# Optimization experiments

Hardware: AMD Instinct MI355X
Metric: run time of the kernel (lower is better)

## Reference

```python
import jax, jax.numpy as jnp
import numpy as np

N_NODES = 15000
N_EDGES = 30000
NUM_GRAPHS = 600
N_STEMS = 6000
N_JBONDS = 3000
DIM = 64
NUM_FEAT = 14
NUM_OUT_PER_STEM = 105


def _lin(a, w, b):
    return a @ w.T + b


def _forward(x, edge_attr, lin0_w, lin0_b, en1_w, en1_b, en2_w, en2_b, root_w, conv_b,
             gru_w_ih, gru_w_hh, gru_b_ih, gru_b_hh, s1_w, s1_b, s2_w, s2_b,
             j1_w, j1_b, j2_w, j2_b, lstm_w_ih, lstm_w_hh, lstm_b_ih, lstm_b_hh,
             lout_w, lout_b, edge_index, stem_atmidx, jbond_atmidx, batch):
    n, dim = x.shape[0], lin0_w.shape[0]
    lrelu = jax.nn.leaky_relu  # negative_slope=0.01 as in torch default
    src, dst = edge_index[0], edge_index[1]

    out = lrelu(_lin(x, lin0_w, lin0_b))
    h = out  # GRU hidden state [N, dim]

    # Edge-conditioned weights (NNConv): small MLP on edge_attr -> [E, dim, dim]
    We = _lin(lrelu(_lin(edge_attr, en1_w, en1_b)), en2_w, en2_b).reshape(-1, dim, dim)
    deg = jnp.clip(jax.ops.segment_sum(jnp.ones_like(dst, dtype=x.dtype), dst, num_segments=n), 1.0)

    for _ in range(6):
        # gather source features, per-edge matvec, scatter-mean to destinations
        msg = jnp.einsum('ei,eio->eo', out[src], We)
        agg = jax.ops.segment_sum(msg, dst, num_segments=n) / deg[:, None]
        m = lrelu(agg + out @ root_w + conv_b)
        # GRUCell (torch gate order: r, z, n)
        gi = _lin(m, gru_w_ih, gru_b_ih)
        gh = _lin(h, gru_w_hh, gru_b_hh)
        ir, iz, inn = jnp.split(gi, 3, axis=-1)
        hr, hz, hn = jnp.split(gh, 3, axis=-1)
        r = jax.nn.sigmoid(ir + hr)
        z = jax.nn.sigmoid(iz + hz)
        ng = jnp.tanh(inn + r * hn)
        h = (1.0 - z) * ng + z * h
        out = h

    stem_preds = _lin(lrelu(_lin(out[stem_atmidx], s1_w, s1_b)), s2_w, s2_b)
    jb = _lin(lrelu(_lin(out[jbond_atmidx.reshape(-1)], j1_w, j1_b)), j2_w, j2_b)
    jbond_preds = jb.reshape(jbond_atmidx.shape).mean(axis=1)

    # Set2Set with 1 processing step (LSTM input 2*dim -> hidden dim)
    b = NUM_GRAPHS
    q_star = jnp.zeros((b, 2 * dim), x.dtype)
    hl = jnp.zeros((b, dim), x.dtype)
    cl = jnp.zeros((b, dim), x.dtype)
    gates = _lin(q_star, lstm_w_ih, lstm_b_ih) + _lin(hl, lstm_w_hh, lstm_b_hh)
    i_, f_, g_, o_ = jnp.split(gates, 4, axis=-1)  # torch LSTM gate order i,f,g,o
    c = jax.nn.sigmoid(f_) * cl + jax.nn.sigmoid(i_) * jnp.tanh(g_)
    q = jax.nn.sigmoid(o_) * jnp.tanh(c)
    e = (out * q[batch]).sum(axis=-1)  # [N]
    emax = jax.ops.segment_max(e, batch, num_segments=b)
    a_un = jnp.exp(e - emax[batch])
    a = a_un / jax.ops.segment_sum(a_un, batch, num_segments=b)[batch]
    r_pool = jax.ops.segment_sum(a[:, None] * out, batch, num_segments=b)
    q_star = jnp.concatenate([q, r_pool], axis=-1)  # [B, 2*dim]

    final = _lin(q_star, lout_w, lout_b)  # [B, 2]
    return final, stem_preds, jbond_preds


def setup_inputs() -> dict:
    key = jax.random.key(0)
    ks = jax.random.split(key, 40)
    d = DIM

    def rn(k, shape, s=0.1):
        return jax.random.normal(k, shape, dtype=jnp.float32) * s

    inp = {}
    inp['x'] = jax.random.normal(ks[0], (N_NODES, NUM_FEAT), dtype=jnp.float32)
    inp['edge_attr'] = jax.random.uniform(ks[1], (N_EDGES, 4), dtype=jnp.float32)
    inp['lin0_w'] = rn(ks[2], (d, NUM_FEAT)); inp['lin0_b'] = rn(ks[3], (d,))
    inp['en1_w'] = rn(ks[4], (d, 4)); inp['en1_b'] = rn(ks[5], (d,))
    inp['en2_w'] = rn(ks[6], (d * d, d), 0.02); inp['en2_b'] = rn(ks[7], (d * d,), 0.02)
    inp['root_w'] = rn(ks[8], (d, d)); inp['conv_b'] = rn(ks[9], (d,))
    inp['gru_w_ih'] = rn(ks[10], (3 * d, d)); inp['gru_w_hh'] = rn(ks[11], (3 * d, d))
    inp['gru_b_ih'] = rn(ks[12], (3 * d,)); inp['gru_b_hh'] = rn(ks[13], (3 * d,))
    inp['s1_w'] = rn(ks[14], (d, d)); inp['s1_b'] = rn(ks[15], (d,))
    inp['s2_w'] = rn(ks[16], (NUM_OUT_PER_STEM, d)); inp['s2_b'] = rn(ks[17], (NUM_OUT_PER_STEM,))
    inp['j1_w'] = rn(ks[18], (d, d)); inp['j1_b'] = rn(ks[19], (d,))
    inp['j2_w'] = rn(ks[20], (1, d)); inp['j2_b'] = rn(ks[21], (1,))
    inp['lstm_w_ih'] = rn(ks[22], (4 * d, 2 * d)); inp['lstm_w_hh'] = rn(ks[23], (4 * d, d))
    inp['lstm_b_ih'] = rn(ks[24], (4 * d,)); inp['lstm_b_hh'] = rn(ks[25], (4 * d,))
    inp['lout_w'] = rn(ks[26], (2, 2 * d)); inp['lout_b'] = rn(ks[27], (2,))
    inp['edge_index'] = jax.random.randint(ks[28], (2, N_EDGES), 0, N_NODES)
    inp['stem_atmidx'] = jax.random.randint(ks[29], (N_STEMS,), 0, N_NODES)
    inp['jbond_atmidx'] = jax.random.randint(ks[30], (N_JBONDS, 2), 0, N_NODES)
    inp['batch'] = jnp.sort(jax.random.randint(ks[31], (N_NODES,), 0, NUM_GRAPHS))
    return inp


def reference(x, edge_attr, lin0_w, lin0_b, en1_w, en1_b, en2_w, en2_b, root_w, conv_b,
              gru_w_ih, gru_w_hh, gru_b_ih, gru_b_hh, s1_w, s1_b, s2_w, s2_b,
              j1_w, j1_b, j2_w, j2_b, lstm_w_ih, lstm_w_hh, lstm_b_ih, lstm_b_hh,
              lout_w, lout_b, edge_index, stem_atmidx, jbond_atmidx, batch):
    return _forward(x, edge_attr, lin0_w, lin0_b, en1_w, en1_b, en2_w, en2_b, root_w, conv_b,
                    gru_w_ih, gru_w_hh, gru_b_ih, gru_b_hh, s1_w, s1_b, s2_w, s2_b,
                    j1_w, j1_b, j2_w, j2_b, lstm_w_ih, lstm_w_hh, lstm_b_ih, lstm_b_hh,
                    lout_w, lout_b, edge_index, stem_atmidx, jbond_atmidx, batch)
```

## Files before the change

### kernel.cpp

```cpp
#include <hip/hip_runtime.h>

typedef unsigned short u16;
typedef unsigned int   u32;

#define N_NODES    15000
#define PADN       15008
#define N_EDGES    30000
#define NUM_GRAPHS 600
#define N_STEMS    6000
#define N_JBONDS   3000

#define OUT_FINAL  0
#define OUT_STEM   1200
#define OUT_JB     631200

#define A1S 68
#define N_CVT 26

#define EBLK 32
#define EGRIDE 938
#define KCH 130
#define A1LS 66
#define RS   66

#define NGROUPS (PADN/16)
#define NWTILES 28
#define HS 72

typedef short frag8 __attribute__((ext_vector_type(8)));
typedef float facc4 __attribute__((ext_vector_type(4)));

__device__ __forceinline__ float u2f(u16 v){ union{u32 i; float f;} c; c.i=((u32)v)<<16; return c.f; }
__device__ __forceinline__ float blo(u32 x){ union{u32 i; float f;} c; c.i=x<<16; return c.f; }
__device__ __forceinline__ float bhi(u32 x){ union{u32 i; float f;} c; c.i=x&0xffff0000u; return c.f; }
__device__ __forceinline__ u16  f2b(float f){ union{float f; u32 u;} c; c.f=f; u32 u=c.u;
                                              return (u16)((u + 0x7fffu + ((u>>16)&1u))>>16); }
__device__ __forceinline__ float lrelu(float x){ return x>0.f ? x : 0.01f*x; }
__device__ __forceinline__ float sigmoidf(float x){ return 1.f/(1.f+expf(-x)); }

__device__ __forceinline__ int lower_bound_i(const int* __restrict__ a, int n, int v){
  int lo=0, hi=n;
  while(lo<hi){ int m=(lo+hi)>>1; if(a[m]<v) lo=m+1; else hi=m; }
  return lo;
}

__device__ __forceinline__ void store_out(void* dout, int isf, int idx, float v){
  if(isf) ((float*)dout)[idx] = v;
  else    ((u16*)dout)[idx]   = f2b(v);
}

__device__ __forceinline__ frag8 pack4(uint4 v, float av){
  union { u32 d[4]; frag8 f; } au;
  u32 dd0 = v.x, dd1 = v.y, dd2 = v.z, dd3 = v.w;
  {
    float plo = blo(dd0)*av, phi = bhi(dd0)*av;
    au.d[0] = __builtin_amdgcn_perm(__float_as_uint(phi)+0x8000u,
                                    __float_as_uint(plo)+0x8000u, 0x07060302u);
  }
  {
    float plo = blo(dd1)*av, phi = bhi(dd1)*av;
    au.d[1] = __builtin_amdgcn_perm(__float_as_uint(phi)+0x8000u,
                                    __float_as_uint(plo)+0x8000u, 0x07060302u);
  }
  {
    float plo = blo(dd2)*av, phi = bhi(dd2)*av;
    au.d[2] = __builtin_amdgcn_perm(__float_as_uint(phi)+0x8000u,
                                    __float_as_uint(plo)+0x8000u, 0x07060302u);
  }
  {
    float plo = blo(dd3)*av, phi = bhi(dd3)*av;
    au.d[3] = __builtin_amdgcn_perm(__float_as_uint(phi)+0x8000u,
                                    __float_as_uint(plo)+0x8000u, 0x07060302u);
  }
  return au.f;
}

__global__ __launch_bounds__(256) void k_sniff(const u16* __restrict__ x, int n, int* __restrict__ flag){
  int i = blockIdx.x*256 + threadIdx.x;
  int local = 0;
  for(; i < n; i += gridDim.x*256){
    u16 v = x[i];
    if(((v>>7)&0xFFu) == 0xFFu) local = 1;
  }
  if(local) atomicOr(flag, 1);
}

struct CvtArgs { const void* src[N_CVT]; float* dst[N_CVT]; int n[N_CVT]; };

__global__ __launch_bounds__(256) void k_cvt(CvtArgs A, const int* __restrict__ flag){
  int isf = *flag;
  int tid = blockIdx.x*256 + threadIdx.x;
  int stride = gridDim.x*256;
  for(int b=0; b<N_CVT; b++){
    int n = A.n[b];
    const float* sf = (const float*)A.src[b];
    const u16*   sb = (const u16*)A.src[b];
    float* d = A.dst[b];
    for(int i=tid; i<n; i+=stride) d[i] = isf ? sf[i] : u2f(sb[i]);
  }
}

__global__ __launch_bounds__(64) void k_lin0(const float* __restrict__ x, const float* __restrict__ w,
                                             const float* __restrict__ b,
                                             float* __restrict__ outF, u16* __restrict__ outB){
  int n = blockIdx.x, o = threadIdx.x;
  __shared__ float xs[14];
  if(o<14) xs[o] = x[n*14+o];
  __syncthreads();
  float acc = b[o];
  #pragma unroll
  for(int i=0;i<14;i++) acc += xs[i]*w[o*14+i];
  float v = lrelu(acc);
  outF[n*64+o] = v;
  outB[n*64+o] = f2b(v);
}

__global__ __launch_bounds__(128) void k_a1(const float* __restrict__ ea,
                                            const float* __restrict__ en1w, const float* __restrict__ en1b,
                                            u16* __restrict__ a1b){
  int e = blockIdx.x, k = threadIdx.x;
  if(k >= A1S) return;
  float v = 0.f;
  if(k < 64){
    float acc = en1b[k];
    #pragma unroll
    for(int c=0;c<4;c++) acc += ea[e*4+c] * en1w[k*4+c];
    v = lrelu(acc);
  } else if(k == 64) v = 1.0f;
  a1b[e*A1S + k] = f2b(v);
}

__global__ __launch_bounds__(256) void k_packW2b(const float* __restrict__ en2w, const float* __restrict__ en2b,
                                                 u16* __restrict__ B2b){
  int idx = blockIdx.x*256 + threadIdx.x;
  if(idx >= KCH*2048) return;
  int jj  = idx & 7;
  int l   = (idx >> 3) & 63;
  int nt  = (idx >> 9) & 3;
  int c   = idx >> 11;
  int q = l >> 4, m16 = l & 15;
  int kidx = c*32 + q*8 + jj;
  int k = kidx >> 6, j = kidx & 63;
  int o = nt*16 + m16;
  float v = (k < 64) ? en2w[((size_t)(j*64 + o))*64 + k] : en2b[j*64 + o];
  B2b[idx] = f2b(v);
}

__global__ __launch_bounds__(256) void k_packNodeW(const float* __restrict__ rootw, const float* __restrict__ wih,
                                                   const float* __restrict__ whh, u16* __restrict__ gBn){
  int idx = blockIdx.x*256 + threadIdx.x;
  if(idx >= NWTILES*4*512) return;
  int jj = idx & 7, l = (idx>>3) & 63, ch = (idx>>9) & 3, t = idx >> 11;
  int m16 = l & 15, q = l >> 4;
  int j = ((ch & 1) ? 32 : 0) + q*8 + jj;
  float v;
  if(t < 4){        int o = t*16 + m16;        v = rootw[j*64 + o]; }
  else if(t < 16){  int g = (t-4)*16 + m16;    v = wih[(size_t)g*64 + j]; }
  else {            int g = (t-16)*16 + m16;   v = whh[(size_t)g*64 + j]; }
  u16 hb = f2b(v);
  gBn[idx] = (ch >> 1) ? f2b(v - u2f(hb)) : hb;
}

__global__ __launch_bounds__(256) void k_packHeads(const float* __restrict__ s1w, const float* __restrict__ s2w,
                                                   const float* __restrict__ j1w,
                                                   float4* __restrict__ s1P, float4* __restrict__ s2P,
                                                   float4* __restrict__ j1P){
  int idx = blockIdx.x*256 + threadIdx.x;
  if(idx < 1024){
    int o = idx & 63, j4 = idx >> 6;
    const float* r = s1w + o*64 + 4*j4;
    s1P[idx] = (float4){r[0], r[1], r[2], r[3]};
    const float* r2 = j1w + o*64 + 4*j4;
    j1P[idx] = (float4){r2[0], r2[1], r2[2], r2[3]};
  }
  if(idx < 1792){
    int j4 = idx / 112, t = idx % 112;
    float4 v = {0.f,0.f,0.f,0.f};
    if(t < 105){
      const float* r = s2w + t*64 + 4*j4;
      v = (float4){r[0], r[1], r[2], r[3]};
    }
    s2P[idx] = v;
  }
}

__global__ __launch_bounds__(256) void k_deg(const int* __restrict__ dst, float* __restrict__ deg){
  int e = blockIdx.x*256 + threadIdx.x;
  if(e < N_EDGES) atomicAdd(&deg[dst[e]], 1.0f);
}

__global__ __launch_bounds__(256, 4) void k_egemm(const u16* __restrict__ outB,
                                               const u16* __restrict__ a1b,
                                               const u16* __restrict__ B2b,
                                               const int* __restrict__ ei,
                                               float* __restrict__ agg){
  int tid = threadIdx.x;
  int l = tid & 63, w = tid >> 6;
  int m16 = l & 15, q = l >> 4;
  int eb = blockIdx.x * EBLK;

  __shared__ __align__(16) u16 a1l[EBLK*A1LS];
  __shared__ __align__(16) float red[4][EBLK*RS];

  int e0 = eb + m16, e1 = eb + 16 + m16;
  int n0 = (e0 < N_EDGES) ? ei[e0] : 0;
  int n1 = (e1 < N_EDGES) ? ei[e1] : 0;
  uint4 o200 = *(const uint4*)(outB + (size_t)n0*64 +      q*8);
  uint4 o201 = *(const uint4*)(outB + (size_t)n0*64 + 32 + q*8);
  uint4 o210 = *(const uint4*)(outB + (size_t)n1*64 +      q*8);
  uint4 o211 = *(const uint4*)(outB + (size_t)n1*64 + 32 + q*8);

  for(int idx = tid; idx < EBLK*33; idx += 256){
    int r = idx / 33, c = idx - r*33;
    int e = eb + r;
    u32 v = (e < N_EDGES) ? ((const u32*)(a1b + (size_t)e*A1S))[c] : 0u;
    ((u32*)a1l)[r*33 + c] = v;
  }
  __syncthreads();

  facc4 acc[2][4];
  #pragma unroll
  for(int t=0;t<2;t++)
    #pragma unroll
    for(int nt=0;nt<4;nt++) acc[t][nt] = (facc4){0.f,0.f,0.f,0.f};

  int ks = (w*65) >> 2, ke = ((w+1)*65) >> 2;
  const frag8* __restrict__ Bg = (const frag8*)B2b;

  frag8 bA[4], bB[4];
  #pragma unroll
  for(int nt=0;nt<4;nt++) bA[nt] = Bg[(size_t)(2*ks)*256 + nt*64 + l];

  for(int k = ks; k < ke; ++k){
    #pragma unroll
    for(int nt=0;nt<4;nt++) bB[nt] = Bg[(size_t)(2*k+1)*256 + nt*64 + l];

    float av0 = u2f(a1l[m16*A1LS + k]);
    float av1 = u2f(a1l[(16+m16)*A1LS + k]);

    {
      frag8 au0 = pack4(o200, av0);
      frag8 au1 = pack4(o210, av1);
      #pragma unroll
      for(int nt=0;nt<4;nt++)
        acc[0][nt] = __builtin_amdgcn_mfma_f32_16x16x32_bf16(au0, bA[nt], acc[0][nt], 0,0,0);
      #pragma unroll
      for(int nt=0;nt<4;nt++)
        acc[1][nt] = __builtin_amdgcn_mfma_f32_16x16x32_bf16(au1, bA[nt], acc[1][nt], 0,0,0);
    }

    int kn = (k+1 < ke) ? (k+1) : k;
    #pragma unroll
    for(int nt=0;nt<4;nt++) bA[nt] = Bg[(size_t)(2*kn)*256 + nt*64 + l];

    {
      frag8 au0 = pack4(o201, av0);
      frag8 au1 = pack4(o211, av1);
      #pragma unroll
      for(int nt=0;nt<4;nt++)
        acc[0][nt] = __builtin_amdgcn_mfma_f32_16x16x32_bf16(au0, bB[nt], acc[0][nt], 0,0,0);
      #pragma unroll
      for(int nt=0;nt<4;nt++)
        acc[1][nt] = __builtin_amdgcn_mfma_f32_16x16x32_bf16(au1, bB[nt], acc[1][nt], 0,0,0);
    }
  }

  #pragma unroll
  for(int t = 0; t < 2; t++){
    #pragma unroll
    for(int nt = 0; nt < 4; nt++){
      #pragma unroll
      for(int r = 0; r < 4; r++){
        int el = t*16 + q*4 + r;
        red[w][el*RS + nt*16 + m16] = acc[t][nt][r];
      }
    }
  }
  __syncthreads();

  for(int i = tid; i < EBLK*64; i += 256){
    int el = i >> 6, o = i & 63;
    int e = eb + el;
    if(e < N_EDGES){
      float s = red[0][el*RS + o] + red[1][el*RS + o]
              + red[2][el*RS + o] + red[3][el*RS + o];
      atomicAdd(&agg[(size_t)ei[N_EDGES + e]*64 + o], s);
    }
  }
}

__global__ __launch_bounds__(256) void k_node(float* __restrict__ agg, const float* __restrict__ deg,
                                              float* __restrict__ outF, u16* __restrict__ outB,
                                              const u16* __restrict__ gBn, const float* __restrict__ convb,
                                              const float* __restrict__ bih, const float* __restrict__ bhh){
  int tid = threadIdx.x;
  int l = tid & 63, w = tid >> 6;
  int m16 = l & 15, q = l >> 4;
  int nb = blockIdx.x * 16;

  __shared__ __align__(16) u16 hhi[16][HS], hlo[16][HS];
  __shared__ __align__(16) u16 mhi[16][HS], mlo[16][HS];

  {
    float4 v = ((const float4*)(outF + (size_t)nb*64))[tid];
    int base = tid*4;
    int node = base >> 6, o = base & 63;
    float vv[4] = {v.x, v.y, v.z, v.w};
    #pragma unroll
    for(int t=0;t<4;t++){
      u16 hb = f2b(vv[t]);
      hhi[node][o+t] = hb;
      hlo[node][o+t] = f2b(vv[t] - u2f(hb));
    }
  }
  __syncthreads();

  const frag8* __restrict__ Bg = (const frag8*)gBn;

#define GEMM6(ACC, A0, A1, L0, L1, T)                                      \
  {                                                                        \
    const frag8* bp = Bg + (size_t)(T)*256 + l;                            \
    frag8 b0 = bp[0], b1 = bp[64], b2 = bp[128], b3 = bp[192];             \
    ACC = __builtin_amdgcn_mfma_f32_16x16x32_bf16(A0, b0, ACC, 0,0,0);     \
    ACC = __builtin_amdgcn_mfma_f32_16x16x32_bf16(A1, b1, ACC, 0,0,0);     \
    ACC = __builtin_amdgcn_mfma_f32_16x16x32_bf16(L0, b0, ACC, 0,0,0);     \
    ACC = __builtin_amdgcn_mfma_f32_16x16x32_bf16(L1, b1, ACC, 0,0,0);     \
    ACC = __builtin_amdgcn_mfma_f32_16x16x32_bf16(A0, b2, ACC, 0,0,0);     \
    ACC = __builtin_amdgcn_mfma_f32_16x16x32_bf16(A1, b3, ACC, 0,0,0);     \
  }

  frag8 hA0 = *(const frag8*)&hhi[m16][q*8];
  frag8 hA1 = *(const frag8*)&hhi[m16][32 + q*8];
  frag8 hL0 = *(const frag8*)&hlo[m16][q*8];
  frag8 hL1 = *(const frag8*)&hlo[m16][32 + q*8];

  facc4 dR  = (facc4){0.f,0.f,0.f,0.f};
  facc4 ghA = (facc4){0.f,0.f,0.f,0.f};
  facc4 ghB = (facc4){0.f,0.f,0.f,0.f};
  facc4 ghC = (facc4){0.f,0.f,0.f,0.f};
  GEMM6(dR,  hA0, hA1, hL0, hL1, w);
  GEMM6(ghA, hA0, hA1, hL0, hL1, 16 + w);
  GEMM6(ghB, hA0, hA1, hL0, hL1, 20 + w);
  GEMM6(ghC, hA0, hA1, hL0, hL1, 24 + w);

  int o = w*16 + m16;
  float cb = convb[o];
  #pragma unroll
  for(int r=0;r<4;r++){
    int node = q*4 + r;
    int n = nb + node;
    float a = agg[(size_t)n*64 + o] / fmaxf(deg[n], 1.0f) + dR[r] + cb;
    agg[(size_t)n*64 + o] = 0.f;
    float mv = lrelu(a);
    u16 mb = f2b(mv);
    mhi[node][o] = mb;
    mlo[node][o] = f2b(mv - u2f(mb));
  }
  __syncthreads();

  frag8 mA0 = *(const frag8*)&mhi[m16][q*8];
  frag8 mA1 = *(const frag8*)&mhi[m16][32 + q*8];
  frag8 mL0 = *(const frag8*)&mlo[m16][q*8];
  frag8 mL1 = *(const frag8*)&mlo[m16][32 + q*8];

  facc4 giA = (facc4){0.f,0.f,0.f,0.f};
  facc4 giB = (facc4){0.f,0.f,0.f,0.f};
  facc4 giC = (facc4){0.f,0.f,0.f,0.f};
  GEMM6(giA, mA0, mA1, mL0, mL1, 4 + w);
  GEMM6(giB, mA0, mA1, mL0, mL1, 8 + w);
  GEMM6(giC, mA0, mA1, mL0, mL1, 12 + w);
#undef GEMM6

  float bi0 = bih[o], bi1 = bih[64+o], bi2 = bih[128+o];
  float bh0 = bhh[o], bh1 = bhh[64+o], bh2 = bhh[128+o];
  #pragma unroll
  for(int r=0;r<4;r++){
    int node = q*4 + r;
    int n = nb + node;
    float ir = giA[r]+bi0, iz = giB[r]+bi1, inn = giC[r]+bi2;
    float hr = ghA[r]+bh0, hz = ghB[r]+bh1, hn = ghC[r]+bh2;
    float rr  = sigmoidf(ir + hr);
    float z   = sigmoidf(iz + hz);
    float ngv = tanhf(inn + rr*hn);
    float hold = u2f(hhi[node][o]) + u2f(hlo[node][o]);
    float hnew = (1.f - z)*ngv + z*hold;
    if(n < N_NODES){
      outF[(size_t)n*64 + o] = hnew;
      outB[(size_t)n*64 + o] = f2b(hnew);
    }
  }
}

__global__ __launch_bounds__(512) void k_stem(const float* __restrict__ outF, const int* __restrict__ sidx,
                                              const float4* __restrict__ s1P, const float* __restrict__ s1b,
                                              const float4* __restrict__ s2P, const float* __restrict__ s2b,
                                              void* __restrict__ dout, const int* __restrict__ flag){
  int grp = threadIdx.x >> 7, t = threadIdx.x & 127;
  int s = blockIdx.x*4 + grp;
  int isf = *flag;
  __shared__ __align__(16) float xs[4][64], hid[4][64];
  int a = sidx[s];
  if(t < 64) xs[grp][t] = outF[(size_t)a*64 + t];
  __syncthreads();
  if(t < 64){
    float acc = s1b[t];
    const float4* xp = (const float4*)xs[grp];
    #pragma unroll 8
    for(int j4=0;j4<16;j4++){
      float4 w = s1P[j4*64+t];
      float4 x = xp[j4];
      acc += w.x*x.x + w.y*x.y + w.z*x.z + w.w*x.w;
    }
    hid[grp][t] = lrelu(acc);
  }
  __syncthreads();
  if(t < 105){
    float acc = s2b[t];
    const float4* hp = (const float4*)hid[grp];
    #pragma unroll 8
    for(int j4=0;j4<16;j4++){
      float4 w = s2P[j4*112+t];
      float4 h = hp[j4];
      acc += w.x*h.x + w.y*h.y + w.z*h.z + w.w*h.w;
    }
    store_out(dout, isf, OUT_STEM + s*105 + t, acc);
  }
}

__global__ __launch_bounds__(512) void k_jbond(const float* __restrict__ outF, const int* __restrict__ jidx,
                                               const float4* __restrict__ j1P, const float* __restrict__ j1b,
                                               const float* __restrict__ j2w, const float* __restrict__ j2b,
                                               void* __restrict__ dout, const int* __restrict__ flag){
  int grp = threadIdx.x >> 7, t = threadIdx.x & 127;
  int jb = blockIdx.x*4 + grp;
  int isf = *flag;
  __shared__ __align__(16) float xs[4][2][64], hid[4][2][64];
  int at = t >> 6, k = t & 63;
  int a = jidx[jb*2 + at];
  xs[grp][at][k] = outF[(size_t)a*64 + k];
  __syncthreads();
  {
    float acc = j1b[k];
    const float4* xp = (const float4*)xs[grp][at];
    #pragma unroll 8
    for(int j4=0;j4<16;j4++){
      float4 w = j1P[j4*64+k];
      float4 x = xp[j4];
      acc += w.x*x.x + w.y*x.y + w.z*x.z + w.w*x.w;
    }
    hid[grp][at][k] = lrelu(acc);
  }
  __syncthreads();
  if(t < 64){
    float p = (hid[grp][0][t] + hid[grp][1][t]) * j2w[t];
    #pragma unroll
    for(int s=32;s;s>>=1) p += __shfl_xor(p, s, 64);
    if(t==0) store_out(dout, isf, OUT_JB + jb, 0.5f*p + j2b[0]);
  }
}

__global__ __launch_bounds__(64) void k_s2s(const float* __restrict__ outF, const int* __restrict__ batch,
                                            const float* __restrict__ bih, const float* __restrict__ bhh,
                                            const float* __restrict__ loutw, const float* __restrict__ loutb,
                                            void* __restrict__ dout, const int* __restrict__ flag){
  int b = blockIdx.x, t = threadIdx.x;
  int isf = *flag;
  float i_ = bih[t]     + bhh[t];
  float g_ = bih[128+t] + bhh[128+t];
  float o_ = bih[192+t] + bhh[192+t];
  float c  = sigmoidf(i_)*tanhf(g_);
  float q  = sigmoidf(o_)*tanhf(c);

  int lo = lower_bound_i(batch, N_NODES, b);
  int hi = lower_bound_i(batch, N_NODES, b+1);

  float emax = -3.4e38f;
  for(int n=lo;n<hi;n++){
    float p = outF[n*64+t]*q;
    #pragma unroll
    for(int s=32;s;s>>=1) p += __shfl_xor(p, s, 64);
    emax = fmaxf(emax, p);
  }
  float Z = 0.f, racc = 0.f;
  for(int n=lo;n<hi;n++){
    float v = outF[n*64+t];
    float p = v*q;
    #pragma unroll
    for(int s=32;s;s>>=1) p += __shfl_xor(p, s, 64);
    float w = expf(p - emax);
    Z += w; racc += w*v;
  }
  float rp = (hi>lo) ? racc/Z : 0.f;

  #pragma unroll
  for(int j=0;j<2;j++){
    float p = q*loutw[j*128+t] + rp*loutw[j*128+64+t];
    #pragma unroll
    for(int s=32;s;s>>=1) p += __shfl_xor(p, s, 64);
    if(t==0) store_out(dout, isf, OUT_FINAL + b*2 + j, p + loutb[j]);
  }
}

extern "C" void kernel_launch(void* const* d_in, const int* in_sizes, int n_in,
                              void* d_out, int out_size, void* d_ws, size_t ws_size,
                              hipStream_t stream) {
  const int* edge_index  = (const int*)d_in[28];
  const int* stem_atmidx = (const int*)d_in[29];
  const int* jbond_atmidx= (const int*)d_in[30];
  const int* batch       = (const int*)d_in[31];

  char* ws = (char*)d_ws;
  size_t off = 0;
  auto alloc = [&](size_t bytes)->void*{ void* p = ws + off; off = (off + bytes + 255) & ~(size_t)255; return p; };

  int*   flag = (int*)  alloc(4);
  float* outF = (float*)alloc((size_t)PADN*64*4);
  u16*   outB = (u16*)  alloc((size_t)PADN*64*2);
  float* agg  = (float*)alloc((size_t)PADN*64*4);
  u16*   a1b  = (u16*)  alloc((size_t)N_EDGES*A1S*2);
  u16*   B2b  = (u16*)  alloc((size_t)KCH*2048*2 + 2048*2);
  u16*   gBn  = (u16*)  alloc((size_t)NWTILES*4*512*2);
  float* deg  = (float*)alloc((size_t)PADN*4);
  float4* s1P   = (float4*)alloc(1024*16);
  float4* s2P   = (float4*)alloc(1792*16);
  float4* j1P   = (float4*)alloc(1024*16);

  static const int cvt_idx[N_CVT] = {0,1,2,3,4,5,6,7,8,9,10,11,12,13,14,15,16,17,18,19,20,21,24,25,26,27};
  CvtArgs A;
  float* cF[N_CVT];
  for(int i=0;i<N_CVT;i++){
    int src = cvt_idx[i];
    int n = in_sizes[src];
    cF[i] = (float*)alloc((size_t)n*4);
    A.src[i] = d_in[src];
    A.dst[i] = cF[i];
    A.n[i]   = n;
  }
  (void)ws_size; (void)n_in; (void)out_size;
  float* xF=cF[0];   float* eaF=cF[1];  float* l0w=cF[2];  float* l0b=cF[3];
  float* e1w=cF[4];  float* e1b=cF[5];  float* e2w=cF[6];  float* e2b=cF[7];
  float* rootw=cF[8];float* convb=cF[9];
  float* wih=cF[10]; float* whh=cF[11]; float* bih=cF[12]; float* bhh=cF[13];
  float* s1w=cF[14]; float* s1b=cF[15]; float* s2w=cF[16]; float* s2b=cF[17];
  float* j1w=cF[18]; float* j1b=cF[19]; float* j2w=cF[20]; float* j2b=cF[21];
  float* lbih=cF[22];float* lbhh=cF[23];float* loutw=cF[24];float* loutb=cF[25];

  hipMemsetAsync(flag, 0, 4, stream);
  hipMemsetAsync(deg,  0, (size_t)PADN*4, stream);
  hipMemsetAsync(outF + (size_t)N_NODES*64, 0, (size_t)(PADN-N_NODES)*64*4, stream);
  hipMemsetAsync(outB + (size_t)N_NODES*64, 0, (size_t)(PADN-N_NODES)*64*2, stream);
  hipMemsetAsync(agg,  0, (size_t)PADN*64*4, stream);

  k_sniff <<<128, 256, 0, stream>>>((const u16*)d_in[0], in_sizes[0], flag);
  k_cvt   <<<512, 256, 0, stream>>>(A, flag);

  k_lin0    <<<N_NODES, 64, 0, stream>>>(xF, l0w, l0b, outF, outB);
  k_a1      <<<N_EDGES, 128, 0, stream>>>(eaF, e1w, e1b, a1b);
  k_packW2b <<<(KCH*2048+255)/256, 256, 0, stream>>>(e2w, e2b, B2b);
  k_packNodeW<<<(NWTILES*4*512+255)/256, 256, 0, stream>>>(rootw, wih, whh, gBn);
  k_packHeads<<<7, 256, 0, stream>>>(s1w, s2w, j1w, s1P, s2P, j1P);
  k_deg     <<<(N_EDGES+255)/256, 256, 0, stream>>>(edge_index + N_EDGES, deg);

  for(int it=0; it<6; it++){
    k_egemm<<<EGRIDE, 256, 0, stream>>>(outB, a1b, B2b, edge_index, agg);
    k_node <<<NGROUPS, 256, 0, stream>>>(agg, deg, outF, outB, gBn, convb, bih, bhh);
  }

  k_stem <<<N_STEMS/4, 512, 0, stream>>>(outF, stem_atmidx, s1P, s1b, s2P, s2b, d_out, flag);
  k_jbond<<<N_JBONDS/4, 512, 0, stream>>>(outF, jbond_atmidx, j1P, j1b, j2w, j2b, d_out, flag);
  k_s2s  <<<NUM_GRAPHS, 64, 0, stream>>>(outF, batch, lbih, lbhh, loutw, loutb, d_out, flag);
}
```

Before: 457.0 us.

## Merge setup kernels and deepen B-fragment prefetch in the edge GEMM

The buffer memsets are folded into the sniff kernel, the degree count is folded into k_a1, and the three weight-packing kernels become one k_packAll launch. Together these cut the number of separate setup launches. In k_egemm the B-fragment prefetch now loads a whole pair of k-steps ahead, so more loads are in flight per MFMA batch. Launch bounds drop from 4 to 3 blocks per CU to leave room for the extra fragment registers, which may lower occupancy.

```diff
diff --git a/kernel.cpp b/kernel.cpp
--- a/kernel.cpp
+++ b/kernel.cpp
@@ -26,6 +26,11 @@
 #define NGROUPS (PADN/16)
 #define NWTILES 28
 #define HS 72
+
+#define PACK_W2B_N (KCH*2048)
+#define PACK_NW_N  (NWTILES*4*512)
+#define PACK_HD_N  1792
+#define PACK_TOTAL (PACK_W2B_N + PACK_NW_N + PACK_HD_N)
 
 typedef short frag8 __attribute__((ext_vector_type(8)));
 typedef float facc4 __attribute__((ext_vector_type(4)));
@@ -75,14 +80,22 @@
   return au.f;
 }
 
-__global__ __launch_bounds__(256) void k_sniff(const u16* __restrict__ x, int n, int* __restrict__ flag){
-  int i = blockIdx.x*256 + threadIdx.x;
+__global__ __launch_bounds__(256) void k_sniff(const u16* __restrict__ x, int n, int* __restrict__ flag,
+                                               float* __restrict__ deg, float* __restrict__ agg,
+                                               float* __restrict__ outF, u16* __restrict__ outB){
+  int tid = blockIdx.x*256 + threadIdx.x;
+  int stride = gridDim.x*256;
   int local = 0;
-  for(; i < n; i += gridDim.x*256){
+  for(int i = tid; i < n; i += stride){
     u16 v = x[i];
     if(((v>>7)&0xFFu) == 0xFFu) local = 1;
   }
   if(local) atomicOr(flag, 1);
+  float4 z = (float4){0.f,0.f,0.f,0.f};
+  for(int i = tid; i < PADN; i += stride) deg[i] = 0.f;
+  for(int i = tid; i < PADN*64/4; i += stride) ((float4*)agg)[i] = z;
+  for(int i = tid; i < (PADN-N_NODES)*64/4; i += stride) ((float4*)(outF + (size_t)N_NODES*64))[i] = z;
+  for(int i = tid; i < (PADN-N_NODES)*64/8; i += stride) ((float4*)(outB + (size_t)N_NODES*64))[i] = z;
 }
 
 struct CvtArgs { const void* src[N_CVT]; float* dst[N_CVT]; int n[N_CVT]; };
@@ -117,7 +130,8 @@
 
 __global__ __launch_bounds__(128) void k_a1(const float* __restrict__ ea,
                                             const float* __restrict__ en1w, const float* __restrict__ en1b,
-                                            u16* __restrict__ a1b){
+                                            u16* __restrict__ a1b,
+                                            const int* __restrict__ ei, float* __restrict__ deg){
   int e = blockIdx.x, k = threadIdx.x;
   if(k >= A1S) return;
   float v = 0.f;
@@ -128,68 +142,66 @@
     v = lrelu(acc);
   } else if(k == 64) v = 1.0f;
   a1b[e*A1S + k] = f2b(v);
-}
-
-__global__ __launch_bounds__(256) void k_packW2b(const float* __restrict__ en2w, const float* __restrict__ en2b,
-                                                 u16* __restrict__ B2b){
+  if(k == 65) atomicAdd(&deg[ei[N_EDGES + e]], 1.0f);
+}
+
+__global__ __launch_bounds__(256) void k_packAll(const float* __restrict__ en2w, const float* __restrict__ en2b,
+                                                 u16* __restrict__ B2b,
+                                                 const float* __restrict__ rootw, const float* __restrict__ wih,
+                                                 const float* __restrict__ whh, u16* __restrict__ gBn,
+                                                 const float* __restrict__ s1w, const float* __restrict__ s2w,
+                                                 const float* __restrict__ j1w,
+                                                 float4* __restrict__ s1P, float4* __restrict__ s2P,
+                                                 float4* __restrict__ j1P){
   int idx = blockIdx.x*256 + threadIdx.x;
-  if(idx >= KCH*2048) return;
-  int jj  = idx & 7;
-  int l   = (idx >> 3) & 63;
-  int nt  = (idx >> 9) & 3;
-  int c   = idx >> 11;
-  int q = l >> 4, m16 = l & 15;
-  int kidx = c*32 + q*8 + jj;
-  int k = kidx >> 6, j = kidx & 63;
-  int o = nt*16 + m16;
-  float v = (k < 64) ? en2w[((size_t)(j*64 + o))*64 + k] : en2b[j*64 + o];
-  B2b[idx] = f2b(v);
-}
-
-__global__ __launch_bounds__(256) void k_packNodeW(const float* __restrict__ rootw, const float* __restrict__ wih,
-                                                   const float* __restrict__ whh, u16* __restrict__ gBn){
-  int idx = blockIdx.x*256 + threadIdx.x;
-  if(idx >= NWTILES*4*512) return;
-  int jj = idx & 7, l = (idx>>3) & 63, ch = (idx>>9) & 3, t = idx >> 11;
-  int m16 = l & 15, q = l >> 4;
-  int j = ((ch & 1) ? 32 : 0) + q*8 + jj;
-  float v;
-  if(t < 4){        int o = t*16 + m16;        v = rootw[j*64 + o]; }
-  else if(t < 16){  int g = (t-4)*16 + m16;    v = wih[(size_t)g*64 + j]; }
-  else {            int g = (t-16)*16 + m16;   v = whh[(size_t)g*64 + j]; }
-  u16 hb = f2b(v);
-  gBn[idx] = (ch >> 1) ? f2b(v - u2f(hb)) : hb;
-}
-
-__global__ __launch_bounds__(256) void k_packHeads(const float* __restrict__ s1w, const float* __restrict__ s2w,
-                                                   const float* __restrict__ j1w,
-                                                   float4* __restrict__ s1P, float4* __restrict__ s2P,
-                                                   float4* __restrict__ j1P){
-  int idx = blockIdx.x*256 + threadIdx.x;
-  if(idx < 1024){
-    int o = idx & 63, j4 = idx >> 6;
-    const float* r = s1w + o*64 + 4*j4;
-    s1P[idx] = (float4){r[0], r[1], r[2], r[3]};
-    const float* r2 = j1w + o*64 + 4*j4;
-    j1P[idx] = (float4){r2[0], r2[1], r2[2], r2[3]};
-  }
-  if(idx < 1792){
-    int j4 = idx / 112, t = idx % 112;
-    float4 v = {0.f,0.f,0.f,0.f};
-    if(t < 105){
-      const float* r = s2w + t*64 + 4*j4;
-      v = (float4){r[0], r[1], r[2], r[3]};
-    }
-    s2P[idx] = v;
-  }
-}
-
-__global__ __launch_bounds__(256) void k_deg(const int* __restrict__ dst, float* __restrict__ deg){
-  int e = blockIdx.x*256 + threadIdx.x;
-  if(e < N_EDGES) atomicAdd(&deg[dst[e]], 1.0f);
-}
-
-__global__ __launch_bounds__(256, 4) void k_egemm(const u16* __restrict__ outB,
+  if(idx < PACK_W2B_N){
+    int jj  = idx & 7;
+    int l   = (idx >> 3) & 63;
+    int nt  = (idx >> 9) & 3;
+    int c   = idx >> 11;
+    int q = l >> 4, m16 = l & 15;
+    int kidx = c*32 + q*8 + jj;
+    int k = kidx >> 6, j = kidx & 63;
+    int o = nt*16 + m16;
+    float v = (k < 64) ? en2w[((size_t)(j*64 + o))*64 + k] : en2b[j*64 + o];
+    B2b[idx] = f2b(v);
+    return;
+  }
+  idx -= PACK_W2B_N;
+  if(idx < PACK_NW_N){
+    int jj = idx & 7, l = (idx>>3) & 63, ch = (idx>>9) & 3, t = idx >> 11;
+    int m16 = l & 15, q = l >> 4;
+    int j = ((ch & 1) ? 32 : 0) + q*8 + jj;
+    float v;
+    if(t < 4){        int o = t*16 + m16;        v = rootw[j*64 + o]; }
+    else if(t < 16){  int g = (t-4)*16 + m16;    v = wih[(size_t)g*64 + j]; }
+    else {            int g = (t-16)*16 + m16;   v = whh[(size_t)g*64 + j]; }
+    u16 hb = f2b(v);
+    gBn[idx] = (ch >> 1) ? f2b(v - u2f(hb)) : hb;
+    return;
+  }
+  idx -= PACK_NW_N;
+  if(idx < PACK_HD_N){
+    if(idx < 1024){
+      int o = idx & 63, j4 = idx >> 6;
+      const float* r = s1w + o*64 + 4*j4;
+      s1P[idx] = (float4){r[0], r[1], r[2], r[3]};
+      const float* r2 = j1w + o*64 + 4*j4;
+      j1P[idx] = (float4){r2[0], r2[1], r2[2], r2[3]};
+    }
+    {
+      int j4 = idx / 112, t = idx % 112;
+      float4 v = {0.f,0.f,0.f,0.f};
+      if(t < 105){
+        const float* r = s2w + t*64 + 4*j4;
+        v = (float4){r[0], r[1], r[2], r[3]};
+      }
+      s2P[idx] = v;
+    }
+  }
+}
+
+__global__ __launch_bounds__(256, 3) void k_egemm(const u16* __restrict__ outB,
                                                const u16* __restrict__ a1b,
                                                const u16* __restrict__ B2b,
                                                const int* __restrict__ ei,
@@ -227,43 +239,56 @@
   int ks = (w*65) >> 2, ke = ((w+1)*65) >> 2;
   const frag8* __restrict__ Bg = (const frag8*)B2b;
 
-  frag8 bA[4], bB[4];
-  #pragma unroll
-  for(int nt=0;nt<4;nt++) bA[nt] = Bg[(size_t)(2*ks)*256 + nt*64 + l];
-
-  for(int k = ks; k < ke; ++k){
-    #pragma unroll
-    for(int nt=0;nt<4;nt++) bB[nt] = Bg[(size_t)(2*k+1)*256 + nt*64 + l];
-
-    float av0 = u2f(a1l[m16*A1LS + k]);
-    float av1 = u2f(a1l[(16+m16)*A1LS + k]);
-
-    {
-      frag8 au0 = pack4(o200, av0);
-      frag8 au1 = pack4(o210, av1);
-      #pragma unroll
-      for(int nt=0;nt<4;nt++)
-        acc[0][nt] = __builtin_amdgcn_mfma_f32_16x16x32_bf16(au0, bA[nt], acc[0][nt], 0,0,0);
-      #pragma unroll
-      for(int nt=0;nt<4;nt++)
-        acc[1][nt] = __builtin_amdgcn_mfma_f32_16x16x32_bf16(au1, bA[nt], acc[1][nt], 0,0,0);
-    }
-
-    int kn = (k+1 < ke) ? (k+1) : k;
-    #pragma unroll
-    for(int nt=0;nt<4;nt++) bA[nt] = Bg[(size_t)(2*kn)*256 + nt*64 + l];
-
-    {
-      frag8 au0 = pack4(o201, av0);
-      frag8 au1 = pack4(o211, av1);
-      #pragma unroll
-      for(int nt=0;nt<4;nt++)
-        acc[0][nt] = __builtin_amdgcn_mfma_f32_16x16x32_bf16(au0, bB[nt], acc[0][nt], 0,0,0);
-      #pragma unroll
-      for(int nt=0;nt<4;nt++)
-        acc[1][nt] = __builtin_amdgcn_mfma_f32_16x16x32_bf16(au1, bB[nt], acc[1][nt], 0,0,0);
-    }
-  }
+  frag8 bE0[4], bO0[4], bE1[4], bO1[4];
+  #pragma unroll
+  for(int nt=0;nt<4;nt++){
+    bE0[nt] = Bg[(size_t)(2*ks  )*256 + nt*64 + l];
+    bO0[nt] = Bg[(size_t)(2*ks+1)*256 + nt*64 + l];
+  }
+
+#define COMPUTE(KK, BE, BO)                                                          \
+  {                                                                                  \
+    float av0 = u2f(a1l[m16*A1LS + (KK)]);                                           \
+    float av1 = u2f(a1l[(16+m16)*A1LS + (KK)]);                                      \
+    {                                                                                \
+      frag8 aE0 = pack4(o200, av0);                                                  \
+      frag8 aE1 = pack4(o210, av1);                                                  \
+      _Pragma("unroll")                                                              \
+      for(int nt=0;nt<4;nt++)                                                        \
+        acc[0][nt] = __builtin_amdgcn_mfma_f32_16x16x32_bf16(aE0, BE[nt], acc[0][nt], 0,0,0); \
+      _Pragma("unroll")                                                              \
+      for(int nt=0;nt<4;nt++)                                                        \
+        acc[1][nt] = __builtin_amdgcn_mfma_f32_16x16x32_bf16(aE1, BE[nt], acc[1][nt], 0,0,0); \
+    }                                                                                \
+    {                                                                                \
+      frag8 aO0 = pack4(o201, av0);                                                  \
+      frag8 aO1 = pack4(o211, av1);                                                  \
+      _Pragma("unroll")                                                              \
+      for(int nt=0;nt<4;nt++)                                                        \
+        acc[0][nt] = __builtin_amdgcn_mfma_f32_16x16x32_bf16(aO0, BO[nt], acc[0][nt], 0,0,0); \
+      _Pragma("unroll")                                                              \
+      for(int nt=0;nt<4;nt++)                                                        \
+        acc[1][nt] = __builtin_amdgcn_mfma_f32_16x16x32_bf16(aO1, BO[nt], acc[1][nt], 0,0,0); \
+    }                                                                                \
+  }
+
+  for(int k = ks; k < ke; k += 2){
+    int k1 = (k+1 < ke) ? k+1 : k;
+    #pragma unroll
+    for(int nt=0;nt<4;nt++){
+      bE1[nt] = Bg[(size_t)(2*k1  )*256 + nt*64 + l];
+      bO1[nt] = Bg[(size_t)(2*k1+1)*256 + nt*64 + l];
+    }
+    COMPUTE(k, bE0, bO0);
+    int k2 = (k+2 < ke) ? k+2 : k;
+    #pragma unroll
+    for(int nt=0;nt<4;nt++){
+      bE0[nt] = Bg[(size_t)(2*k2  )*256 + nt*64 + l];
+      bO0[nt] = Bg[(size_t)(2*k2+1)*256 + nt*64 + l];
+    }
+    if(k+1 < ke) COMPUTE(k+1, bE1, bO1);
+  }
+#undef COMPUTE
 
   #pragma unroll
   for(int t = 0; t < 2; t++){
@@ -546,20 +571,14 @@
   float* lbih=cF[22];float* lbhh=cF[23];float* loutw=cF[24];float* loutb=cF[25];
 
   hipMemsetAsync(flag, 0, 4, stream);
-  hipMemsetAsync(deg,  0, (size_t)PADN*4, stream);
-  hipMemsetAsync(outF + (size_t)N_NODES*64, 0, (size_t)(PADN-N_NODES)*64*4, stream);
-  hipMemsetAsync(outB + (size_t)N_NODES*64, 0, (size_t)(PADN-N_NODES)*64*2, stream);
-  hipMemsetAsync(agg,  0, (size_t)PADN*64*4, stream);
-
-  k_sniff <<<128, 256, 0, stream>>>((const u16*)d_in[0], in_sizes[0], flag);
+
+  k_sniff <<<128, 256, 0, stream>>>((const u16*)d_in[0], in_sizes[0], flag, deg, agg, outF, outB);
   k_cvt   <<<512, 256, 0, stream>>>(A, flag);
 
   k_lin0    <<<N_NODES, 64, 0, stream>>>(xF, l0w, l0b, outF, outB);
-  k_a1      <<<N_EDGES, 128, 0, stream>>>(eaF, e1w, e1b, a1b);
-  k_packW2b <<<(KCH*2048+255)/256, 256, 0, stream>>>(e2w, e2b, B2b);
-  k_packNodeW<<<(NWTILES*4*512+255)/256, 256, 0, stream>>>(rootw, wih, whh, gBn);
-  k_packHeads<<<7, 256, 0, stream>>>(s1w, s2w, j1w, s1P, s2P, j1P);
-  k_deg     <<<(N_EDGES+255)/256, 256, 0, stream>>>(edge_index + N_EDGES, deg);
+  k_a1      <<<N_EDGES, 128, 0, stream>>>(eaF, e1w, e1b, a1b, edge_index, deg);
+  k_packAll <<<PACK_TOTAL/256, 256, 0, stream>>>(e2w, e2b, B2b, rootw, wih, whh, gBn,
+                                                 s1w, s2w, j1w, s1P, s2P, j1P);
 
   for(int it=0; it<6; it++){
     k_egemm<<<EGRIDE, 256, 0, stream>>>(outB, a1b, B2b, edge_index, agg);
```

Measured after the change: 458.6 us. Within noise of the previous version (+0.4%).
